# Performance work log

Hardware: AMD Instinct MI355X
Metric: run time of the kernel (lower is better)

The kernel has to match this reference:

```python
import jax, jax.numpy as jnp
import numpy as np

DIM = 1024
N_HEADS = 16
HEAD_DIM = DIM // N_HEADS


def setup_inputs() -> dict:
    key = jax.random.key(0)
    k_x, k_qkv_w, k_qkv_b, k_p_w, k_p_b = jax.random.split(key, 5)
    s = 1.0 / np.sqrt(DIM)
    return {
        "x": jax.random.normal(k_x, (2, 2048, DIM), dtype=jnp.float32),
        # stored as [in, out] so forward is x @ W + b (equivalent to torch Linear)
        "qkv_w": jax.random.uniform(k_qkv_w, (DIM, 3 * DIM), minval=-s, maxval=s, dtype=jnp.float32),
        "qkv_b": jax.random.uniform(k_qkv_b, (3 * DIM,), minval=-s, maxval=s, dtype=jnp.float32),
        "proj_w": jax.random.uniform(k_p_w, (DIM, DIM), minval=-s, maxval=s, dtype=jnp.float32),
        "proj_b": jax.random.uniform(k_p_b, (DIM,), minval=-s, maxval=s, dtype=jnp.float32),
    }


def reference(x, qkv_w, qkv_b, proj_w, proj_b):
    b, s, _ = x.shape
    qkv = x @ qkv_w + qkv_b                       # [b, s, 3*dim]
    q, k, v = jnp.split(qkv, 3, axis=-1)
    def split_heads(t):
        return t.reshape(b, s, N_HEADS, HEAD_DIM).transpose(0, 2, 1, 3)  # [b, h, s, d]
    q, k, v = map(split_heads, (q, k, v))
    scale = 1.0 / np.sqrt(HEAD_DIM)
    scores = jnp.einsum("bhqd,bhkd->bhqk", q, k) * scale
    attn = jax.nn.softmax(scores, axis=-1)
    out = jnp.einsum("bhqk,bhkd->bhqd", attn, v)
    out = out.transpose(0, 2, 1, 3).reshape(b, s, DIM)
    return out @ proj_w + proj_b
```

## Files before the change

### kernel.cpp

```cpp
#include <hip/hip_runtime.h>
#include <hip/hip_bf16.h>

typedef __attribute__((ext_vector_type(8))) short bf16x8;
typedef __attribute__((ext_vector_type(4))) float f32x4;
typedef __attribute__((ext_vector_type(16))) float f32x16;
typedef __attribute__((ext_vector_type(4))) unsigned short u16x4;
typedef __attribute__((ext_vector_type(8))) unsigned short u16x8v;

#define S_LEN 2048
#define NHEAD 16
#define HDIM 64
#define DIM 1024

__device__ __forceinline__ unsigned short f2bf(float f) {
    union { float f; unsigned u; } x; x.f = f;
    unsigned r = x.u + 0x7FFFu + ((x.u >> 16) & 1u);
    return (unsigned short)(r >> 16);
}
__device__ __forceinline__ unsigned short f2bf_fast(float f) {
    union { float f; unsigned u; } x; x.f = f;
    return (unsigned short)((x.u + 0x8000u) >> 16);
}

__device__ __forceinline__ f32x4 mfma16(bf16x8 a, bf16x8 b, f32x4 c) {
    return __builtin_amdgcn_mfma_f32_16x16x32_bf16(a, b, c, 0, 0, 0);
}
__device__ __forceinline__ f32x16 mfma32(bf16x8 a, bf16x8 b, f32x16 c) {
    return __builtin_amdgcn_mfma_f32_32x32x16_bf16(a, b, c, 0, 0, 0);
}

__device__ __forceinline__ float fexp2(float x) {
#if __has_builtin(__builtin_amdgcn_exp2f)
    return __builtin_amdgcn_exp2f(x);
#else
    return exp2f(x);
#endif
}

__device__ __forceinline__ void gl_lds16(const void* g, void* l) {
    __builtin_amdgcn_global_load_lds(
        (const __attribute__((address_space(1))) unsigned int*)g,
        (__attribute__((address_space(3))) unsigned int*)l, 16, 0, 0);
}

__device__ __forceinline__ void wtrans_body(const float* __restrict__ W,
                                            unsigned short* __restrict__ Wt,
                                            int K, int N, int k0, int n0,
                                            float (*lds)[65], int tid) {
    for (int idx = tid; idx < 1024; idx += 256) {
        int row = idx >> 4, c = (idx & 15) << 2;
        float4 v = *reinterpret_cast<const float4*>(&W[(size_t)(k0 + row) * N + n0 + c]);
        lds[row][c] = v.x; lds[row][c + 1] = v.y; lds[row][c + 2] = v.z; lds[row][c + 3] = v.w;
    }
    __syncthreads();
    for (int idx = tid; idx < 1024; idx += 256) {
        int row = idx >> 4, c = (idx & 15) << 2;
        u16x4 o;
        o[0] = f2bf(lds[c][row]);     o[1] = f2bf(lds[c + 1][row]);
        o[2] = f2bf(lds[c + 2][row]); o[3] = f2bf(lds[c + 3][row]);
        *reinterpret_cast<u16x4*>(&Wt[(size_t)(n0 + row) * K + k0 + c]) = o;
    }
}

__global__ __launch_bounds__(256) void prep_kernel(const float* __restrict__ X,
                                                   unsigned short* __restrict__ Xb,
                                                   const float* __restrict__ Wq,
                                                   unsigned short* __restrict__ Wqt,
                                                   const float* __restrict__ Wp,
                                                   unsigned short* __restrict__ Wpt) {
    __shared__ float lds[64][65];
    const int b = blockIdx.x, tid = threadIdx.x;
    if (b < 2048) {
        size_t i = ((size_t)b * 256 + tid) * 8;
        float4 a = *reinterpret_cast<const float4*>(&X[i]);
        float4 c = *reinterpret_cast<const float4*>(&X[i + 4]);
        u16x8v o;
        o[0] = f2bf(a.x); o[1] = f2bf(a.y); o[2] = f2bf(a.z); o[3] = f2bf(a.w);
        o[4] = f2bf(c.x); o[5] = f2bf(c.y); o[6] = f2bf(c.z); o[7] = f2bf(c.w);
        *reinterpret_cast<u16x8v*>(&Xb[i]) = o;
    } else if (b < 2816) {
        int idx = b - 2048;
        wtrans_body(Wq, Wqt, 1024, 3072, (idx & 15) * 64, (idx >> 4) * 64, lds, tid);
    } else {
        int idx = b - 2816;
        wtrans_body(Wp, Wpt, 1024, 1024, (idx & 15) * 64, (idx >> 4) * 64, lds, tid);
    }
}

template <int MODE>
__global__ __launch_bounds__(512) void gemm_kernel(
    const unsigned short* __restrict__ Ab, const unsigned short* __restrict__ Bt,
    const float* __restrict__ bias,
    unsigned short* __restrict__ Qb, unsigned short* __restrict__ Kb,
    unsigned short* __restrict__ Vt, float* __restrict__ outf) {
    __shared__ unsigned short Alds[128 * 64];
    __shared__ unsigned short Blds[128 * 64];
    const int tid = threadIdx.x;
    const int m0 = blockIdx.x * 128, n0 = blockIdx.y * 128;
    const int wid = tid >> 6, lane = tid & 63;
    const int wm = wid >> 2, wn = wid & 3;
    const int lr = lane & 15, lg = lane >> 4;

    const char* Abase = (const char*)(Ab + (size_t)m0 * 1024);
    const char* Bbase = (const char*)(Bt + (size_t)n0 * 1024);

    int srcOff[2], dstOff[2];
#pragma unroll
    for (int i = 0; i < 2; ++i) {
        int off = i * 8192 + tid * 16;
        int row = off >> 7, col = off & 127;
        srcOff[i] = row * 2048 + (col ^ ((row & 7) << 4));
        dstOff[i] = off;
    }
    const int swz = (lr & 7) << 4;

    f32x4 acc[4][2] = {};

    for (int kt = 0; kt < 16; ++kt) {
        __syncthreads();
#pragma unroll
        for (int i = 0; i < 2; ++i) {
            gl_lds16(Abase + srcOff[i] + kt * 128, (char*)Alds + dstOff[i]);
            gl_lds16(Bbase + srcOff[i] + kt * 128, (char*)Blds + dstOff[i]);
        }
        __syncthreads();

#pragma unroll
        for (int ks = 0; ks < 2; ++ks) {
            bf16x8 af[4], bfr[2];
#pragma unroll
            for (int i = 0; i < 4; ++i)
                af[i] = *reinterpret_cast<const bf16x8*>(
                    (const char*)Alds + (wm * 64 + i * 16 + lr) * 128 + ((ks * 64 + lg * 16) ^ swz));
#pragma unroll
            for (int j = 0; j < 2; ++j)
                bfr[j] = *reinterpret_cast<const bf16x8*>(
                    (const char*)Blds + (wn * 32 + j * 16 + lr) * 128 + ((ks * 64 + lg * 16) ^ swz));
            __builtin_amdgcn_s_setprio(1);
#pragma unroll
            for (int i = 0; i < 4; ++i)
#pragma unroll
                for (int j = 0; j < 2; ++j)
                    acc[i][j] = mfma16(af[i], bfr[j], acc[i][j]);
            __builtin_amdgcn_s_setprio(0);
        }
    }

    if constexpr (MODE == 0) {
        const int sec = n0 >> 10;
#pragma unroll
        for (int j = 0; j < 2; ++j) {
            int gn = n0 + wn * 32 + j * 16 + lr;
            float bv = bias[gn];
            int nn = gn & 1023, h = nn >> 6, d = nn & 63;
            if (sec == 2) {
#pragma unroll
                for (int i = 0; i < 4; ++i) {
                    int sb = m0 + wm * 64 + i * 16 + lg * 4;
                    size_t bhv = (size_t)((sb >> 11) * NHEAD + h);
                    u16x4 pv;
#pragma unroll
                    for (int r = 0; r < 4; ++r) pv[r] = f2bf(acc[i][j][r] + bv);
                    *reinterpret_cast<u16x4*>(&Vt[(bhv * HDIM + d) * S_LEN + (sb & 2047)]) = pv;
                }
            } else {
#pragma unroll
                for (int i = 0; i < 4; ++i) {
#pragma unroll
                    for (int r = 0; r < 4; ++r) {
                        int m = m0 + wm * 64 + i * 16 + lg * 4 + r;
                        int b_ = m >> 11, s_ = m & 2047;
                        size_t bh = (size_t)(b_ * NHEAD + h);
                        float v = acc[i][j][r] + bv;
                        if (sec == 0)
                            Qb[(bh * S_LEN + s_) * HDIM + d] = f2bf(v * 0.18033688f);
                        else
                            Kb[(bh * S_LEN + s_) * HDIM + d] = f2bf(v);
                    }
                }
            }
        }
    } else {
#pragma unroll
        for (int j = 0; j < 2; ++j) {
            int gn = n0 + wn * 32 + j * 16 + lr;
            float bv = bias[gn];
#pragma unroll
            for (int i = 0; i < 4; ++i) {
#pragma unroll
                for (int r = 0; r < 4; ++r) {
                    int m = m0 + wm * 64 + i * 16 + lg * 4 + r;
                    outf[(size_t)m * DIM + gn] = acc[i][j][r] + bv;
                }
            }
        }
    }
}

__device__ __forceinline__ void repack32(const f32x16& p, bf16x8 (&pa)[2]) {
#pragma unroll
    for (int k2 = 0; k2 < 2; ++k2) {
        const int rb = 8 * k2;
        unsigned aw[2], bw[2];
#pragma unroll
        for (int u = 0; u < 2; ++u) {
            unsigned a, b;
            asm("v_cvt_pk_bf16_f32 %0, %1, %2"
                : "=v"(a) : "v"(p[rb + 2 * u]), "v"(p[rb + 2 * u + 1]));
            asm("v_cvt_pk_bf16_f32 %0, %1, %2"
                : "=v"(b) : "v"(p[rb + 4 + 2 * u]), "v"(p[rb + 4 + 2 * u + 1]));
            asm volatile("v_permlane32_swap_b32 %0, %1" : "+v"(a), "+v"(b));
            aw[u] = a; bw[u] = b;
        }
        union { unsigned w[4]; bf16x8 v; } pu;
        pu.w[0] = aw[0]; pu.w[1] = aw[1]; pu.w[2] = bw[0]; pu.w[3] = bw[1];
        pa[k2] = pu.v;
    }
}

#define NT64 32
__global__ __launch_bounds__(512, 4) void attn_kernel(const unsigned short* __restrict__ Qb,
                                                      const unsigned short* __restrict__ Kb,
                                                      const unsigned short* __restrict__ Vt,
                                                      unsigned short* __restrict__ Ob) {
    __shared__ char smem[3 * 16384 + 512];
    const int L = blockIdx.x;
    const int xcd = L & 7, slot = L >> 3;
    const int bh = xcd + 8 * (slot & 3);
    const int qblk = slot >> 2;
    const int wid = threadIdx.x >> 6;
    const int lane = threadIdx.x & 63;
    const int l31 = lane & 31, hi = lane >> 5;
    const int qs = wid & 3, kh = wid >> 2;
    const int q0 = qblk * 128 + qs * 32;

    const unsigned short* qrow = &Qb[((size_t)bh * S_LEN + q0 + l31) * HDIM];
    bf16x8 qf[4];
#pragma unroll
    for (int kst = 0; kst < 4; ++kst)
        qf[kst] = *reinterpret_cast<const bf16x8*>(&qrow[kst * 16 + hi * 8]);

    bf16x8 onesf;
#pragma unroll
    for (int j = 0; j < 8; ++j) onesf[j] = (short)0x3F80;

    const char* kT = (const char*)&Kb[(size_t)bh * S_LEN * HDIM];
    const char* vT = (const char*)&Vt[(size_t)bh * HDIM * S_LEN];

    const char* sbase = (wid < 4) ? kT : vT;
    const int tileStride = (wid < 4) ? 8192 : 128;
    int srcOff[2], dstOff[2];
#pragma unroll
    for (int i = 0; i < 2; ++i) {
        int id = 2 * wid + i;
        if (id < 8) {
            int khs = (id >> 2) & 1, kst = id & 3;
            srcOff[i] = (khs * 32 + l31) * 128 + kst * 32 + hi * 16;
        } else {
            int c = id - 8;
            int khs = (c >> 2) & 1, dt = (c >> 1) & 1, k2 = c & 1;
            srcOff[i] = (dt * 32 + l31) * 4096 + khs * 64 + k2 * 32 + hi * 16;
        }
        dstOff[i] = id * 1024;
    }

    f32x16 acc[2] = {};
    f32x16 sacc = {};

#pragma unroll
    for (int i = 0; i < 2; ++i)
        gl_lds16(sbase + srcOff[i], smem + dstOff[i]);
#pragma unroll
    for (int i = 0; i < 2; ++i)
        gl_lds16(sbase + tileStride + srcOff[i], smem + 16384 + dstOff[i]);
    asm volatile("s_waitcnt vmcnt(2)" ::: "memory");
    __builtin_amdgcn_s_barrier();

    const int cofs = kh * 4096;
    for (int t = 0; t < NT64; ++t) {
        const char* bufb = smem + (t % 3) * 16384;
        const char* kbb = bufb + cofs + lane * 16;
        const char* vbb = bufb + 8192 + cofs + lane * 16;

        f32x16 p = {};
        __builtin_amdgcn_s_setprio(1);
#pragma unroll
        for (int kst = 0; kst < 4; ++kst) {
            bf16x8 kb = *reinterpret_cast<const bf16x8*>(kbb + kst * 1024);
            p = mfma32(kb, qf[kst], p);
        }
        __builtin_amdgcn_s_setprio(0);

#pragma unroll
        for (int r = 0; r < 16; ++r) p[r] = fexp2(p[r]);
        bf16x8 pa[2];
        repack32(p, pa);

        __builtin_amdgcn_s_setprio(1);
        sacc = mfma32(pa[0], onesf, sacc);
        sacc = mfma32(pa[1], onesf, sacc);
#pragma unroll
        for (int dt = 0; dt < 2; ++dt)
#pragma unroll
            for (int k2 = 0; k2 < 2; ++k2) {
                bf16x8 vb = *reinterpret_cast<const bf16x8*>(vbb + (dt * 2 + k2) * 1024);
                acc[dt] = mfma32(pa[k2], vb, acc[dt]);
            }
        __builtin_amdgcn_s_setprio(0);

        if (t + 2 < NT64) {
            char* nb = smem + ((t + 2) % 3) * 16384;
#pragma unroll
            for (int i = 0; i < 2; ++i)
                gl_lds16(sbase + (size_t)(t + 2) * tileStride + srcOff[i], nb + dstOff[i]);
            asm volatile("s_waitcnt vmcnt(2)" ::: "memory");
            __builtin_amdgcn_s_barrier();
        } else if (t + 1 < NT64) {
            asm volatile("s_waitcnt vmcnt(0)" ::: "memory");
            __builtin_amdgcn_s_barrier();
        }
    }

    __syncthreads();

    float* cacc = (float*)smem;
    float* cls  = (float*)(smem + 49152);
    if (kh == 1) {
#pragma unroll
        for (int dt = 0; dt < 2; ++dt)
#pragma unroll
            for (int r = 0; r < 16; ++r)
                cacc[qs * 2048 + dt * 1024 + r * 64 + lane] = acc[dt][r];
        if (l31 == 0) {
#pragma unroll
            for (int r = 0; r < 16; ++r) {
                int rq = (r & 3) + 8 * (r >> 2) + 4 * hi;
                cls[qs * 32 + rq] = sacc[r];
            }
        }
    }
    __syncthreads();
    if (kh == 0) {
#pragma unroll
        for (int dt = 0; dt < 2; ++dt)
#pragma unroll
            for (int r = 0; r < 16; ++r)
                acc[dt][r] += cacc[qs * 2048 + dt * 1024 + r * 64 + lane];

        const int b_ = bh >> 4, h = bh & 15;
        float inv[16];
#pragma unroll
        for (int r = 0; r < 16; ++r) {
            int rq = (r & 3) + 8 * (r >> 2) + 4 * hi;
            inv[r] = 1.f / (sacc[r] + cls[qs * 32 + rq]);
        }
#pragma unroll
        for (int dt = 0; dt < 2; ++dt)
#pragma unroll
            for (int r = 0; r < 16; ++r) {
                int rq = (r & 3) + 8 * (r >> 2) + 4 * hi;
                int q = q0 + rq;
                Ob[((size_t)(b_ * S_LEN + q)) * DIM + h * HDIM + dt * 32 + l31] =
                    f2bf_fast(acc[dt][r] * inv[r]);
            }
    }
}

extern "C" void kernel_launch(void* const* d_in, const int* in_sizes, int n_in,
                              void* d_out, int out_size, void* d_ws, size_t ws_size,
                              hipStream_t stream) {
    const float* x      = (const float*)d_in[0];
    const float* qkv_w  = (const float*)d_in[1];
    const float* qkv_b  = (const float*)d_in[2];
    const float* proj_w = (const float*)d_in[3];
    const float* proj_b = (const float*)d_in[4];
    float* out = (float*)d_out;

    unsigned short* Wqkvt = (unsigned short*)d_ws;
    unsigned short* Wpt   = Wqkvt + 3072 * 1024;
    unsigned short* Qb    = Wpt + 1024 * 1024;
    unsigned short* Kb    = Qb + 32 * 2048 * 64;
    unsigned short* Vt    = Kb + 32 * 2048 * 64;
    unsigned short* Ob    = Vt + 32 * 2048 * 64;
    unsigned short* Xb    = Ob + 4096 * 1024;

    prep_kernel<<<3072, 256, 0, stream>>>(x, Xb, qkv_w, Wqkvt, proj_w, Wpt);

    gemm_kernel<0><<<dim3(32, 24), 512, 0, stream>>>(Xb, Wqkvt, qkv_b, Qb, Kb, Vt, nullptr);
    attn_kernel<<<512, 512, 0, stream>>>(Qb, Kb, Vt, Ob);
    gemm_kernel<1><<<dim3(32, 8), 512, 0, stream>>>(Ob, Wpt, proj_b, nullptr, nullptr, nullptr, out);
}
```

Before: 108.4 us.

## Double-buffer LDS tiles in projection GEMM to overlap global loads with MFMA

Turns the GEMM kernel's single LDS buffers into two, prefetches two K-tiles up front, and issues the load for tile kt+2 into the buffer just consumed. It uses explicit vmcnt waits and raw barriers so global-to-LDS copies overlap with MFMA compute instead of stalling each iteration. LDS use doubles to 64KB per block, which may lower occupancy, and the hand-placed waitcnt ordering must be right for correctness.

Result: faster. 104.3 us (median of 2 runs) (-3.8%).

```diff
diff --git a/kernel.cpp b/kernel.cpp
--- a/kernel.cpp
+++ b/kernel.cpp
@@ -93,8 +93,8 @@
     const float* __restrict__ bias,
     unsigned short* __restrict__ Qb, unsigned short* __restrict__ Kb,
     unsigned short* __restrict__ Vt, float* __restrict__ outf) {
-    __shared__ unsigned short Alds[128 * 64];
-    __shared__ unsigned short Blds[128 * 64];
+    __shared__ unsigned short Alds[2][128 * 64];
+    __shared__ unsigned short Blds[2][128 * 64];
     const int tid = threadIdx.x;
     const int m0 = blockIdx.x * 128, n0 = blockIdx.y * 128;
     const int wid = tid >> 6, lane = tid & 63;
@@ -116,26 +116,32 @@
 
     f32x4 acc[4][2] = {};
 
+#pragma unroll
+    for (int i = 0; i < 2; ++i) {
+        gl_lds16(Abase + srcOff[i], (char*)Alds[0] + dstOff[i]);
+        gl_lds16(Bbase + srcOff[i], (char*)Blds[0] + dstOff[i]);
+    }
+#pragma unroll
+    for (int i = 0; i < 2; ++i) {
+        gl_lds16(Abase + srcOff[i] + 128, (char*)Alds[1] + dstOff[i]);
+        gl_lds16(Bbase + srcOff[i] + 128, (char*)Blds[1] + dstOff[i]);
+    }
+    asm volatile("s_waitcnt vmcnt(4)" ::: "memory");
+    __builtin_amdgcn_s_barrier();
+
     for (int kt = 0; kt < 16; ++kt) {
-        __syncthreads();
-#pragma unroll
-        for (int i = 0; i < 2; ++i) {
-            gl_lds16(Abase + srcOff[i] + kt * 128, (char*)Alds + dstOff[i]);
-            gl_lds16(Bbase + srcOff[i] + kt * 128, (char*)Blds + dstOff[i]);
-        }
-        __syncthreads();
-
+        const int cb = kt & 1;
 #pragma unroll
         for (int ks = 0; ks < 2; ++ks) {
             bf16x8 af[4], bfr[2];
 #pragma unroll
             for (int i = 0; i < 4; ++i)
                 af[i] = *reinterpret_cast<const bf16x8*>(
-                    (const char*)Alds + (wm * 64 + i * 16 + lr) * 128 + ((ks * 64 + lg * 16) ^ swz));
+                    (const char*)Alds[cb] + (wm * 64 + i * 16 + lr) * 128 + ((ks * 64 + lg * 16) ^ swz));
 #pragma unroll
             for (int j = 0; j < 2; ++j)
                 bfr[j] = *reinterpret_cast<const bf16x8*>(
-                    (const char*)Blds + (wn * 32 + j * 16 + lr) * 128 + ((ks * 64 + lg * 16) ^ swz));
+                    (const char*)Blds[cb] + (wn * 32 + j * 16 + lr) * 128 + ((ks * 64 + lg * 16) ^ swz));
             __builtin_amdgcn_s_setprio(1);
 #pragma unroll
             for (int i = 0; i < 4; ++i)
@@ -143,6 +149,20 @@
                 for (int j = 0; j < 2; ++j)
                     acc[i][j] = mfma16(af[i], bfr[j], acc[i][j]);
             __builtin_amdgcn_s_setprio(0);
+        }
+        if (kt + 1 < 16) {
+            __builtin_amdgcn_s_barrier();
+            if (kt + 2 < 16) {
+#pragma unroll
+                for (int i = 0; i < 2; ++i) {
+                    gl_lds16(Abase + srcOff[i] + (kt + 2) * 128, (char*)Alds[cb] + dstOff[i]);
+                    gl_lds16(Bbase + srcOff[i] + (kt + 2) * 128, (char*)Blds[cb] + dstOff[i]);
+                }
+                asm volatile("s_waitcnt vmcnt(4)" ::: "memory");
+            } else {
+                asm volatile("s_waitcnt vmcnt(0)" ::: "memory");
+            }
+            __builtin_amdgcn_s_barrier();
         }
     }
 
```
